# Performance work log

Measured on AMD Instinct MI355X. Metric: run time of the kernel, lower is better.

## Reference

```python
import jax, jax.numpy as jnp
import numpy as np

N, E = 50000, 800000
IN_CH, EDGE_DIM, H, C = 256, 32, 4, 32


def setup_inputs() -> dict:
    key = jax.random.key(0)
    ks = jax.random.split(key, 9)
    inp = {
        "x": jax.random.normal(ks[0], (N, IN_CH), dtype=jnp.float32),
        "edge_index": jax.random.randint(ks[1], (2, E), 0, N, dtype=jnp.int64),
        "edge_attr": jax.random.normal(ks[2], (E, EDGE_DIM), dtype=jnp.float32),
        "dist_weight": jax.random.uniform(ks[3], (E,), dtype=jnp.float32),
        # learned parameters (xavier-ish scale)
        "W_src": jax.random.normal(ks[4], (IN_CH, H * C), dtype=jnp.float32) * (1.0 / np.sqrt(IN_CH)),
        "W_dst": jax.random.normal(ks[5], (IN_CH, H * C), dtype=jnp.float32) * (1.0 / np.sqrt(IN_CH)),
        "W_edge": jax.random.normal(ks[6], (EDGE_DIM, H * C), dtype=jnp.float32) * (1.0 / np.sqrt(EDGE_DIM)),
        "att": jax.random.normal(ks[7], (1, H, C), dtype=jnp.float32) * 0.1,
        "spatial_scale": jnp.ones((H,), dtype=jnp.float32),
    }
    return inp


def reference(x, edge_index, edge_attr, dist_weight, W_src, W_dst, W_edge, att, spatial_scale):
    n = x.shape[0]
    h, c = att.shape[1], att.shape[2]
    src, dst = edge_index[0], edge_index[1]

    x_src = (x @ W_src).reshape(n, h, c)          # [N,H,C]
    x_dst = (x @ W_dst).reshape(n, h, c)          # [N,H,C]
    e_feat = (edge_attr @ W_edge).reshape(-1, h, c)  # [E,H,C]

    # edge-wise attention logits
    alpha = jnp.tanh(x_src[src] + x_dst[dst] + e_feat)  # [E,H,C]
    alpha = jnp.sum(alpha * att, axis=-1)               # [E,H]
    alpha_raw = alpha

    # spatial decay: dist_weight ** spatial_scale per head
    alpha = alpha * dist_weight[:, None] ** spatial_scale[None, :]

    # segment softmax over dst (numerically stable; max is grad-neutral)
    m = jax.ops.segment_max(alpha, dst, num_segments=n)  # [N,H]
    m = jnp.where(jnp.isfinite(m), m, 0.0)               # empty segments -> 0 (matches torch init)
    m = jax.lax.stop_gradient(m)
    ea = jnp.exp(alpha - m[dst])                         # [E,H]
    s = jax.ops.segment_sum(ea, dst, num_segments=n)     # [N,H]
    alpha_norm = ea / (s[dst] + 1e-8)                    # [E,H]

    # weighted aggregation of source features
    msg = x_src[src] * alpha_norm[:, :, None]            # [E,H,C]
    out = jax.ops.segment_sum(msg, dst, num_segments=n)  # [N,H,C]
    return out.reshape(n, h * c), alpha_norm, alpha_raw
```

## Files before the change

kernel.cpp:

```cpp
#include <hip/hip_runtime.h>
#include <hip/hip_bf16.h>

#define N_NODES 50000
#define N_EDGES 800000
#define IN_CH   256
#define EDGE_DIM 32
#define NH 4
#define NC 32
#define HC 128
#define SCAN_BLKS 196
#define EGROUPS (N_EDGES / 64)

typedef __attribute__((ext_vector_type(8))) short bf16x8;
typedef __attribute__((ext_vector_type(4))) float f32x4;

__device__ int g_bsum[256];
__device__ int g_boffs[256];

__device__ __forceinline__ float fexp2(float x) { return __builtin_amdgcn_exp2f(x); }
__device__ __forceinline__ float flog2(float x) { return __builtin_amdgcn_logf(x); }
__device__ __forceinline__ float fexp(float x)  { return __builtin_amdgcn_exp2f(x * 1.44269504089f); }

__device__ __forceinline__ float ftanh(float x) {
    const float e = fexp2(x * 2.88539008178f);
    return 1.0f - 2.0f * __builtin_amdgcn_rcpf(e + 1.0f);
}

__device__ __forceinline__ unsigned short f2bf(float f) {
    union { float f; unsigned int u; } v; v.f = f;
    const unsigned int r = v.u + 0x7fffu + ((v.u >> 16) & 1u);
    return (unsigned short)(r >> 16);
}

__device__ __forceinline__ float ldf(const void* p, long i, bool f32) {
    return f32 ? ((const float*)p)[i]
               : __bfloat162float(((const __hip_bfloat16*)p)[i]);
}

__device__ __forceinline__ int ld_src(const int* ei, long e, bool idx64) {
    return idx64 ? ei[2 * e] : ei[e];
}
__device__ __forceinline__ int ld_dst(const int* ei, long e, bool idx64) {
    return idx64 ? ei[2 * ((long)N_EDGES + e)] : ei[(long)N_EDGES + e];
}

__global__ __launch_bounds__(256) void detect_k(const unsigned short* __restrict__ xu,
                                                const int* __restrict__ ei,
                                                int* __restrict__ flag) {
    __shared__ int zc, bc, nz_idx;
    if (threadIdx.x == 0) { zc = 0; bc = 0; nz_idx = 0; }
    __syncthreads();
    int z = 0, b = 0, hi = 0;
    for (int i = threadIdx.x; i < 16384; i += 256) {
        const unsigned short w = xu[2 * i];
        if (w == 0) ++z;
        if ((w & 0x7F80) == 0x7F80) ++b;
    }
    for (int i = threadIdx.x; i < 8192; i += 256)
        if (ei[2 * i + 1] != 0) hi = 1;
    atomicAdd(&zc, z);
    atomicAdd(&bc, b);
    if (hi) atomicAdd(&nz_idx, 1);
    __syncthreads();
    if (threadIdx.x == 0) {
        flag[0] = (zc > 8192 || bc > 0) ? 1 : 0;
        flag[1] = (nz_idx == 0) ? 1 : 0;
    }
}

__global__ __launch_bounds__(256) void zero_deg_k(int* __restrict__ deg) {
    const int i = blockIdx.x * 256 + threadIdx.x;
    if (i < N_NODES) deg[i] = 0;
}

__global__ __launch_bounds__(256) void hist_k(const int* __restrict__ ei,
                                              const int* __restrict__ flag,
                                              int* __restrict__ deg) {
    const bool idx64 = (flag[1] != 0);
    const long e = (long)blockIdx.x * 256 + threadIdx.x;
    if (e < N_EDGES) atomicAdd(&deg[ld_dst(ei, e, idx64)], 1);
}

__global__ __launch_bounds__(256) void scan1_k(const int* __restrict__ deg,
                                               int* __restrict__ row_ptr) {
    __shared__ int wsum[4];
    const int tid = threadIdx.x;
    const int lane = tid & 63, wid = tid >> 6;
    const int i = blockIdx.x * 256 + tid;
    const int v = (i < N_NODES) ? deg[i] : 0;
    int x = v;
    #pragma unroll
    for (int off = 1; off < 64; off <<= 1) {
        const int t = __shfl_up(x, off);
        if (lane >= off) x += t;
    }
    if (lane == 63) wsum[wid] = x;
    __syncthreads();
    int wpre = 0;
    for (int w = 0; w < wid; ++w) wpre += wsum[w];
    if (i < N_NODES) row_ptr[i] = wpre + x - v;
    if (tid == 0) g_bsum[blockIdx.x] = wsum[0] + wsum[1] + wsum[2] + wsum[3];
}

__global__ __launch_bounds__(256) void scan2_k(int* __restrict__ row_ptr) {
    __shared__ int wsum[4];
    const int tid = threadIdx.x;
    const int lane = tid & 63, wid = tid >> 6;
    const int v = (tid < SCAN_BLKS) ? g_bsum[tid] : 0;
    int x = v;
    #pragma unroll
    for (int off = 1; off < 64; off <<= 1) {
        const int t = __shfl_up(x, off);
        if (lane >= off) x += t;
    }
    if (lane == 63) wsum[wid] = x;
    __syncthreads();
    int wpre = 0;
    for (int w = 0; w < wid; ++w) wpre += wsum[w];
    if (tid < SCAN_BLKS) g_boffs[tid] = wpre + x - v;
    if (tid == 0) row_ptr[N_NODES] = N_EDGES;
}

__global__ __launch_bounds__(256) void scan3_k(int* __restrict__ row_ptr,
                                               int* __restrict__ cursor) {
    const int i = blockIdx.x * 256 + threadIdx.x;
    if (i < N_NODES) {
        const int t = row_ptr[i] + g_boffs[blockIdx.x];
        row_ptr[i] = t;
        cursor[i] = t;
    }
}

__global__ __launch_bounds__(256) void scatter_k(const int* __restrict__ ei,
                                                 const int* __restrict__ flag,
                                                 int* __restrict__ cursor,
                                                 int* __restrict__ eids,
                                                 int* __restrict__ esrc) {
    const bool idx64 = (flag[1] != 0);
    const long e = (long)blockIdx.x * 256 + threadIdx.x;
    if (e >= N_EDGES) return;
    const int dst = ld_dst(ei, e, idx64);
    const int src = ld_src(ei, e, idx64);
    const int pos = atomicAdd(&cursor[dst], 1);
    eids[pos] = (int)e;
    esrc[pos] = src;
}

__global__ __launch_bounds__(256) void node_gemm_k(const void* __restrict__ x,
                                                   const void* __restrict__ Wsrc,
                                                   const void* __restrict__ Wdst,
                                                   const int* __restrict__ flag,
                                                   float* __restrict__ xsrc,
                                                   float* __restrict__ xdst) {
    const bool f32 = (flag[0] != 0);
    __shared__ float sx[8][IN_CH];
    const int tid = threadIdx.x;
    const long n0 = (long)blockIdx.x * 8;
    #pragma unroll
    for (int r = 0; r < 8; ++r)
        sx[r][tid] = ldf(x, (n0 + r) * IN_CH + tid, f32);
    __syncthreads();

    const int mat = tid >> 7;
    const int col = tid & 127;
    const void* __restrict__ W = mat ? Wdst : Wsrc;
    float acc[8] = {0,0,0,0,0,0,0,0};
    for (int k = 0; k < IN_CH; k += 4) {
        const float w0 = ldf(W, (long)(k + 0) * HC + col, f32);
        const float w1 = ldf(W, (long)(k + 1) * HC + col, f32);
        const float w2 = ldf(W, (long)(k + 2) * HC + col, f32);
        const float w3 = ldf(W, (long)(k + 3) * HC + col, f32);
        #pragma unroll
        for (int r = 0; r < 8; ++r) {
            const float4 sv = *(const float4*)&sx[r][k];
            acc[r] += sv.x * w0 + sv.y * w1 + sv.z * w2 + sv.w * w3;
        }
    }
    float* __restrict__ o = mat ? xdst : xsrc;
    #pragma unroll
    for (int r = 0; r < 8; ++r)
        o[(n0 + r) * HC + col] = acc[r];
}

__global__ __launch_bounds__(256) void edge_alpha_k(const int* __restrict__ ei,
                                                    const void* __restrict__ eattr,
                                                    const void* __restrict__ dw,
                                                    const void* __restrict__ Wedge,
                                                    const void* __restrict__ att,
                                                    const void* __restrict__ sscale,
                                                    const int* __restrict__ flag,
                                                    const float* __restrict__ xsrc,
                                                    const float* __restrict__ xdst,
                                                    float* __restrict__ ea_ws,
                                                    float* __restrict__ araw_out) {
    const bool f32   = (flag[0] != 0);
    const bool idx64 = (flag[1] != 0);
    __shared__ int   sSrc[4][16];
    __shared__ int   sDst[4][16];
    __shared__ float sDw[4][16];

    const int tid = threadIdx.x;
    const int l   = tid & 63;
    const int wid = tid >> 6;
    const int jj  = l & 15;
    const int hi  = l >> 4;

    bf16x8 bfrag[8];
    #pragma unroll
    for (int t = 0; t < 8; ++t) {
        union { unsigned short u[8]; bf16x8 v; } bu;
        #pragma unroll
        for (int i = 0; i < 8; ++i) {
            const int k = hi * 8 + i;
            const int col = t * 16 + jj;
            if (f32) bu.u[i] = f2bf(((const float*)Wedge)[k * HC + col]);
            else     bu.u[i] = ((const unsigned short*)Wedge)[k * HC + col];
        }
        bfrag[t] = bu.v;
    }
    float attv[8];
    #pragma unroll
    for (int t = 0; t < 8; ++t) attv[t] = ldf(att, t * 16 + jj, f32);
    const float ssv = ldf(sscale, l & 3, f32);

    for (long g = blockIdx.x; g < EGROUPS; g += (long)gridDim.x) {
        const long e0 = g * 64 + (long)wid * 16;

        if (l < 16)      sSrc[wid][l]      = ld_src(ei, e0 + l, idx64);
        else if (l < 32) sDst[wid][l - 16] = ld_dst(ei, e0 + (l - 16), idx64);
        else if (l < 48) sDw[wid][l - 32]  = ldf(dw, e0 + (l - 32), f32);
        __builtin_amdgcn_wave_barrier();

        bf16x8 afrag;
        if (f32) {
            const float* ar = (const float*)eattr + (e0 + jj) * EDGE_DIM + hi * 8;
            const float4 p0 = *(const float4*)ar;
            const float4 p1 = *(const float4*)(ar + 4);
            union { unsigned short u[8]; bf16x8 v; } au;
            au.u[0] = f2bf(p0.x); au.u[1] = f2bf(p0.y); au.u[2] = f2bf(p0.z); au.u[3] = f2bf(p0.w);
            au.u[4] = f2bf(p1.x); au.u[5] = f2bf(p1.y); au.u[6] = f2bf(p1.z); au.u[7] = f2bf(p1.w);
            afrag = au.v;
        } else {
            afrag = *(const bf16x8*)((const unsigned short*)eattr + (e0 + jj) * EDGE_DIM + hi * 8);
        }

        const f32x4 zero = {0.f, 0.f, 0.f, 0.f};
        f32x4 acc[8];
        #pragma unroll
        for (int t = 0; t < 8; ++t)
            acc[t] = __builtin_amdgcn_mfma_f32_16x16x32_bf16(afrag, bfrag[t], zero, 0, 0, 0);

        float hsum[4][4] = {{0,0,0,0},{0,0,0,0},{0,0,0,0},{0,0,0,0}};
        #pragma unroll
        for (int r = 0; r < 4; ++r) {
            const int sI = sSrc[wid][hi * 4 + r];
            const int dI = sDst[wid][hi * 4 + r];
            const float* bs = xsrc + (long)sI * HC + jj;
            const float* bd = xdst + (long)dI * HC + jj;
            float xsv[8], xdv[8];
            #pragma unroll
            for (int t = 0; t < 8; ++t) xsv[t] = bs[t * 16];
            #pragma unroll
            for (int t = 0; t < 8; ++t) xdv[t] = bd[t * 16];
            #pragma unroll
            for (int t = 0; t < 8; ++t) {
                const float v = ftanh(acc[t][r] + xsv[t] + xdv[t]) * attv[t];
                hsum[r][t >> 1] += v;
            }
        }

        #pragma unroll
        for (int r = 0; r < 4; ++r)
            #pragma unroll
            for (int h2 = 0; h2 < 4; ++h2) {
                float v = hsum[r][h2];
                v += __shfl_xor(v, 1);
                v += __shfl_xor(v, 2);
                v += __shfl_xor(v, 4);
                v += __shfl_xor(v, 8);
                hsum[r][h2] = v;
            }

        float val = hsum[0][0];
        #pragma unroll
        for (int r = 0; r < 4; ++r)
            #pragma unroll
            for (int h2 = 0; h2 < 4; ++h2)
                if (jj == r * 4 + h2) val = hsum[r][h2];

        const int r_sel = jj >> 2;
        const long er = e0 + hi * 4 + r_sel;
        const float dwv = sDw[wid][hi * 4 + r_sel];
        araw_out[er * 4 + (jj & 3)] = val;
        const float d = fexp2(ssv * flog2(dwv));
        ea_ws[er * 4 + (jj & 3)] = fexp(val * d);
        __builtin_amdgcn_wave_barrier();
    }
}

__global__ __launch_bounds__(256) void aggregate_k(const int* __restrict__ row_ptr,
                                                   const int* __restrict__ eids,
                                                   const int* __restrict__ esrc,
                                                   const float* __restrict__ ea_ws,
                                                   const float* __restrict__ xsrc,
                                                   float* __restrict__ s_ws,
                                                   float* __restrict__ out) {
    const int tid = threadIdx.x;
    const int lane = tid & 63;
    const int n = blockIdx.x * 4 + (tid >> 6);
    if (n >= N_NODES) return;
    const int h = lane >> 4;

    const int p0 = row_ptr[n];
    const int p1 = row_ptr[n + 1];

    float ax = 0.0f, ay = 0.0f, sa = 0.0f;
    for (int p = p0; p < p1; ++p) {
        const int e = eids[p];
        const int src = esrc[p];
        const float w = ea_ws[(long)e * 4 + h];
        const float2 xv = *(const float2*)(xsrc + (long)src * HC + (lane << 1));
        ax += w * xv.x;
        ay += w * xv.y;
        sa += w;
    }
    const float inv = 1.0f / (sa + 1e-8f);
    float* o = out + (long)n * HC + (lane << 1);
    o[0] = ax * inv;
    o[1] = ay * inv;
    if ((lane & 15) == 0) s_ws[(long)n * 4 + h] = sa;
}

__global__ __launch_bounds__(256) void edge_norm_k(const int* __restrict__ ei,
                                                   const int* __restrict__ flag,
                                                   const float* __restrict__ ea_ws,
                                                   const float* __restrict__ s_ws,
                                                   float* __restrict__ anorm) {
    const bool idx64 = (flag[1] != 0);
    const long i = (long)blockIdx.x * 256 + threadIdx.x;
    if (i >= (long)N_EDGES * NH) return;
    const long e = i >> 2;
    const int h = (int)(i & 3);
    const int dst = ld_dst(ei, e, idx64);
    anorm[i] = ea_ws[i] / (s_ws[(long)dst * 4 + h] + 1e-8f);
}

extern "C" void kernel_launch(void* const* d_in, const int* in_sizes, int n_in,
                              void* d_out, int out_size, void* d_ws, size_t ws_size,
                              hipStream_t stream) {
    const void* x      = d_in[0];
    const int*  ei     = (const int*)d_in[1];
    const void* eattr  = d_in[2];
    const void* dw     = d_in[3];
    const void* Wsrc   = d_in[4];
    const void* Wdst   = d_in[5];
    const void* Wedge  = d_in[6];
    const void* att    = d_in[7];
    const void* sscale = d_in[8];

    float* out   = (float*)d_out;
    float* anorm = out + (long)N_NODES * HC;
    float* araw  = anorm + (long)N_EDGES * NH;

    float* ws      = (float*)d_ws;
    int*   flag    = (int*)d_ws;
    float* xsrc    = ws + 64;
    float* xdst    = xsrc + (long)N_NODES * HC;
    float* ea      = xdst + (long)N_NODES * HC;
    float* s_ws    = ea + (long)N_EDGES * NH;
    int*   deg     = (int*)(s_ws + (long)N_NODES * NH);
    int*   row_ptr = deg + N_NODES;
    int*   cursor  = row_ptr + N_NODES + 1;
    int*   eids    = cursor + N_NODES;
    int*   esrc    = eids + N_EDGES;

    detect_k<<<1, 256, 0, stream>>>((const unsigned short*)x, ei, flag);
    zero_deg_k<<<(N_NODES + 255) / 256, 256, 0, stream>>>(deg);
    hist_k<<<(N_EDGES + 255) / 256, 256, 0, stream>>>(ei, flag, deg);
    scan1_k<<<SCAN_BLKS, 256, 0, stream>>>(deg, row_ptr);
    scan2_k<<<1, 256, 0, stream>>>(row_ptr);
    scan3_k<<<SCAN_BLKS, 256, 0, stream>>>(row_ptr, cursor);
    scatter_k<<<(N_EDGES + 255) / 256, 256, 0, stream>>>(ei, flag, cursor, eids, esrc);
    node_gemm_k<<<N_NODES / 8, 256, 0, stream>>>(x, Wsrc, Wdst, flag, xsrc, xdst);
    edge_alpha_k<<<2048, 256, 0, stream>>>(ei, eattr, dw, Wedge, att, sscale,
                                           flag, xsrc, xdst, ea, araw);
    aggregate_k<<<(N_NODES + 3) / 4, 256, 0, stream>>>(row_ptr, eids, esrc, ea, xsrc, s_ws, out);
    edge_norm_k<<<((long)N_EDGES * NH + 255) / 256, 256, 0, stream>>>(ei, flag, ea, s_ws, anorm);
}
```

Before: 734.8 us.

## Add bf16 MFMA node GEMM path with a separate f32 fallback kernel

Splits the node projection GEMM into two kernels selected at runtime by the dtype flag. The bf16 path keeps the W fragments in registers and uses 16x16x32 bf16 MFMA over 16-node tiles with a grid-stride loop. The f32 kernel drops the per-load dtype branch and reads floats directly. Both kernels are always launched and one exits early, so whichever path is inactive still costs an extra launch.

```diff
diff --git a/kernel.cpp b/kernel.cpp
--- a/kernel.cpp
+++ b/kernel.cpp
@@ -10,6 +10,7 @@
 #define HC 128
 #define SCAN_BLKS 196
 #define EGROUPS (N_EDGES / 64)
+#define NTILES (N_NODES / 16)
 
 typedef __attribute__((ext_vector_type(8))) short bf16x8;
 typedef __attribute__((ext_vector_type(4))) float f32x4;
@@ -146,30 +147,86 @@
     esrc[pos] = src;
 }
 
-__global__ __launch_bounds__(256) void node_gemm_k(const void* __restrict__ x,
-                                                   const void* __restrict__ Wsrc,
-                                                   const void* __restrict__ Wdst,
-                                                   const int* __restrict__ flag,
-                                                   float* __restrict__ xsrc,
-                                                   float* __restrict__ xdst) {
-    const bool f32 = (flag[0] != 0);
+__global__ __launch_bounds__(256) void node_gemm_mfma_k(const unsigned short* __restrict__ x,
+                                                        const unsigned short* __restrict__ Wsrc,
+                                                        const unsigned short* __restrict__ Wdst,
+                                                        const int* __restrict__ flag,
+                                                        float* __restrict__ xsrc,
+                                                        float* __restrict__ xdst) {
+    if (flag[0] != 0) return;
+    const int tid = threadIdx.x;
+    const int l   = tid & 63;
+    const int w   = tid >> 6;
+    const int jj  = l & 15;
+    const int hi  = l >> 4;
+    const int cbase = w * 64;
+
+    bf16x8 bfrag[8][4];
+    #pragma unroll
+    for (int ks = 0; ks < 8; ++ks)
+        #pragma unroll
+        for (int t = 0; t < 4; ++t) {
+            const int c = cbase + t * 16 + jj;
+            const unsigned short* Wp = (c < HC) ? (Wsrc + c) : (Wdst + (c - HC));
+            union { unsigned short u[8]; bf16x8 v; } bu;
+            #pragma unroll
+            for (int i = 0; i < 8; ++i)
+                bu.u[i] = Wp[(ks * 32 + hi * 8 + i) * HC];
+            bfrag[ks][t] = bu.v;
+        }
+
+    for (int nt = blockIdx.x; nt < NTILES; nt += gridDim.x) {
+        const long n0 = (long)nt * 16;
+        const unsigned short* xr = x + (n0 + jj) * IN_CH + hi * 8;
+        bf16x8 afrag[8];
+        #pragma unroll
+        for (int ks = 0; ks < 8; ++ks)
+            afrag[ks] = *(const bf16x8*)(xr + ks * 32);
+
+        f32x4 acc[4];
+        #pragma unroll
+        for (int t = 0; t < 4; ++t) acc[t] = (f32x4){0.f, 0.f, 0.f, 0.f};
+        #pragma unroll
+        for (int ks = 0; ks < 8; ++ks)
+            #pragma unroll
+            for (int t = 0; t < 4; ++t)
+                acc[t] = __builtin_amdgcn_mfma_f32_16x16x32_bf16(afrag[ks], bfrag[ks][t], acc[t], 0, 0, 0);
+
+        #pragma unroll
+        for (int t = 0; t < 4; ++t) {
+            const int c = cbase + t * 16 + jj;
+            float* obase = (c < HC) ? (xsrc + c) : (xdst + (c - HC));
+            #pragma unroll
+            for (int r = 0; r < 4; ++r)
+                obase[(n0 + hi * 4 + r) * HC] = acc[t][r];
+        }
+    }
+}
+
+__global__ __launch_bounds__(256) void node_gemm_f32_k(const void* __restrict__ x,
+                                                       const void* __restrict__ Wsrc,
+                                                       const void* __restrict__ Wdst,
+                                                       const int* __restrict__ flag,
+                                                       float* __restrict__ xsrc,
+                                                       float* __restrict__ xdst) {
+    if (flag[0] == 0) return;
     __shared__ float sx[8][IN_CH];
     const int tid = threadIdx.x;
     const long n0 = (long)blockIdx.x * 8;
     #pragma unroll
     for (int r = 0; r < 8; ++r)
-        sx[r][tid] = ldf(x, (n0 + r) * IN_CH + tid, f32);
+        sx[r][tid] = ((const float*)x)[(n0 + r) * IN_CH + tid];
     __syncthreads();
 
     const int mat = tid >> 7;
     const int col = tid & 127;
-    const void* __restrict__ W = mat ? Wdst : Wsrc;
+    const float* __restrict__ W = (const float*)(mat ? Wdst : Wsrc);
     float acc[8] = {0,0,0,0,0,0,0,0};
     for (int k = 0; k < IN_CH; k += 4) {
-        const float w0 = ldf(W, (long)(k + 0) * HC + col, f32);
-        const float w1 = ldf(W, (long)(k + 1) * HC + col, f32);
-        const float w2 = ldf(W, (long)(k + 2) * HC + col, f32);
-        const float w3 = ldf(W, (long)(k + 3) * HC + col, f32);
+        const float w0 = W[(long)(k + 0) * HC + col];
+        const float w1 = W[(long)(k + 1) * HC + col];
+        const float w2 = W[(long)(k + 2) * HC + col];
+        const float w3 = W[(long)(k + 3) * HC + col];
         #pragma unroll
         for (int r = 0; r < 8; ++r) {
             const float4 sv = *(const float4*)&sx[r][k];
@@ -381,7 +438,11 @@
     scan2_k<<<1, 256, 0, stream>>>(row_ptr);
     scan3_k<<<SCAN_BLKS, 256, 0, stream>>>(row_ptr, cursor);
     scatter_k<<<(N_EDGES + 255) / 256, 256, 0, stream>>>(ei, flag, cursor, eids, esrc);
-    node_gemm_k<<<N_NODES / 8, 256, 0, stream>>>(x, Wsrc, Wdst, flag, xsrc, xdst);
+    node_gemm_mfma_k<<<1024, 256, 0, stream>>>((const unsigned short*)x,
+                                               (const unsigned short*)Wsrc,
+                                               (const unsigned short*)Wdst,
+                                               flag, xsrc, xdst);
+    node_gemm_f32_k<<<N_NODES / 8, 256, 0, stream>>>(x, Wsrc, Wdst, flag, xsrc, xdst);
     edge_alpha_k<<<2048, 256, 0, stream>>>(ei, eattr, dw, Wedge, att, sscale,
                                            flag, xsrc, xdst, ea, araw);
     aggregate_k<<<(N_NODES + 3) / 4, 256, 0, stream>>>(row_ptr, eids, esrc, ea, xsrc, s_ws, out);
```

Result: no change. 729.7 us (-0.7%).
